# Kernel tuning notes

Measured on AMD Instinct MI355X. Metric: run time of the kernel, lower is better.

## Reference

```python
import jax, jax.numpy as jnp
import numpy as np

N_SEND = 49152   # 12 * 64^2 HEALPix nodes
N_REC = 65536    # 256x256 receiver grid
N_EDGES = 262144 # N_REC * 4 nearest senders
D_MODEL = 256
EDGE_IN, EDGE_OUT = 4, 64
LIN_IN, LIN_OUT = 320, 256
B = 2


def setup_inputs() -> dict:
    key = jax.random.key(0)
    ks = jax.random.split(key, 8)
    x = jax.random.normal(ks[0], (B, N_SEND, D_MODEL), dtype=jnp.float32)
    senders = jax.random.randint(ks[1], (N_EDGES,), 0, N_SEND, dtype=jnp.int32)
    receivers = jax.random.randint(ks[2], (N_EDGES,), 0, N_REC, dtype=jnp.int32)
    edge_index = jnp.stack([senders, receivers], axis=0)
    edge_attr = jax.random.normal(ks[3], (N_EDGES, EDGE_IN), dtype=jnp.float32)
    s = lambda fan_in: 1.0 / np.sqrt(fan_in)
    return {
        "x": x,
        "edge_index": edge_index,
        "edge_attr": edge_attr,
        "ee_w1": jax.random.normal(ks[4], (EDGE_IN, EDGE_OUT), dtype=jnp.float32) * s(EDGE_IN),
        "ee_b1": jnp.zeros((EDGE_OUT,), dtype=jnp.float32),
        "ee_w2": jax.random.normal(ks[5], (EDGE_OUT, EDGE_OUT), dtype=jnp.float32) * s(EDGE_OUT),
        "ee_b2": jnp.zeros((EDGE_OUT,), dtype=jnp.float32),
        "ff_w1": jax.random.normal(ks[6], (LIN_IN, LIN_OUT), dtype=jnp.float32) * s(LIN_IN),
        "ff_b1": jnp.zeros((LIN_OUT,), dtype=jnp.float32),
        "ff_w2": jax.random.normal(ks[7], (LIN_OUT, LIN_OUT), dtype=jnp.float32) * s(LIN_OUT),
        "ff_b2": jnp.zeros((LIN_OUT,), dtype=jnp.float32),
    }


def reference(x, edge_index, edge_attr,
              ee_w1, ee_b1, ee_w2, ee_b2,
              ff_w1, ff_b1, ff_w2, ff_b2):
    senders, receivers = edge_index[0], edge_index[1]
    # edge embedder MLP: [E, edge_in] -> [E, edge_out]
    h = jax.nn.relu(edge_attr @ ee_w1 + ee_b1)
    edge_feat = h @ ee_w2 + ee_b2                       # [E, edge_out]
    # gather sender node features: [B, E, d_model]
    v_s = x[:, senders, :]
    # concat with broadcast edge features: [B, E, d_model + edge_out]
    ef = jnp.broadcast_to(edge_feat[None], (x.shape[0],) + edge_feat.shape)
    v_s_prime = jnp.concatenate([v_s, ef], axis=-1)
    # scatter-sum onto receiver nodes: [B, n_rec, lin_in]
    v_m_sum = jnp.zeros((x.shape[0], N_REC, v_s_prime.shape[-1]), dtype=x.dtype)
    v_m_sum = v_m_sum.at[:, receivers, :].add(v_s_prime)
    # g2m feedforward: [B, n_rec, lin_out]
    h2 = jax.nn.relu(v_m_sum @ ff_w1 + ff_b1)
    return h2 @ ff_w2 + ff_b2
```

## Files before the change

### kernel.cpp

```cpp
#include <hip/hip_runtime.h>
#include <hip/hip_bf16.h>

#define N_SEND 49152
#define N_REC  65536
#define N_EDGES 262144
#define D_MODEL 256
#define EDGE_IN 4
#define EDGE_OUT 64
#define LIN_IN 320
#define LIN_OUT 256
#define BATCH 2

#define GBM 64

typedef __attribute__((ext_vector_type(4))) float f32x4;
typedef __attribute__((ext_vector_type(8))) short bf16x8;

static __device__ __forceinline__ unsigned short f2bf(float f) {
    union { float f; unsigned u; } v; v.f = f;
    unsigned r = v.u + 0x7FFF + ((v.u >> 16) & 1);
    return (unsigned short)(r >> 16);
}
static __device__ __forceinline__ float bf2f(unsigned short h) {
    union { unsigned u; float f; } v; v.u = ((unsigned)h) << 16; return v.f;
}

static __device__ __forceinline__ void async_copy16(void* lds_ptr, const void* g_ptr) {
    __builtin_amdgcn_global_load_lds(
        (const __attribute__((address_space(1))) void*)g_ptr,
        (__attribute__((address_space(3))) void*)lds_ptr, 16, 0, 0);
}

__global__ __launch_bounds__(256) void prep_fused(
    const float* __restrict__ x, unsigned short* __restrict__ xb, int nconv,
    const int* __restrict__ receivers, const float* __restrict__ edge_attr,
    const float* __restrict__ ee_w1, const float* __restrict__ ee_b1,
    const float* __restrict__ ee_w2, const float* __restrict__ ee_b2,
    unsigned short* __restrict__ efs, int* __restrict__ counts,
    const float* __restrict__ w1, const float* __restrict__ w2,
    unsigned short* __restrict__ w1t, unsigned short* __restrict__ w2t)
{
    __shared__ __align__(16) unsigned short h_lds[256 * EDGE_OUT];

    const int bid = blockIdx.x;
    const int tid = threadIdx.x;

    if (bid < nconv) {
        const size_t i = ((size_t)bid * 256 + tid) * 8;
        const float4 v0 = *(const float4*)&x[i];
        const float4 v1 = *(const float4*)&x[i + 4];
        bf16x8 o;
        o[0] = (short)f2bf(v0.x); o[1] = (short)f2bf(v0.y);
        o[2] = (short)f2bf(v0.z); o[3] = (short)f2bf(v0.w);
        o[4] = (short)f2bf(v1.x); o[5] = (short)f2bf(v1.y);
        o[6] = (short)f2bf(v1.z); o[7] = (short)f2bf(v1.w);
        *(bf16x8*)&xb[i] = o;
        return;
    }
    const int b2 = bid - nconv;

    if (b2 < N_EDGES / 256) {
        const int e0 = b2 * 256;
        atomicAdd(&counts[receivers[e0 + tid]], 1);

        {
            const float4 ea = *(const float4*)&edge_attr[(size_t)(e0 + tid) * EDGE_IN];
#pragma unroll
            for (int kb = 0; kb < 8; ++kb) {
                bf16x8 hv;
#pragma unroll
                for (int j = 0; j < 8; ++j) {
                    const int k = kb * 8 + j;
                    float a = ee_b1[k];
                    a += ea.x * ee_w1[0 * EDGE_OUT + k];
                    a += ea.y * ee_w1[1 * EDGE_OUT + k];
                    a += ea.z * ee_w1[2 * EDGE_OUT + k];
                    a += ea.w * ee_w1[3 * EDGE_OUT + k];
                    hv[j] = (short)f2bf(fmaxf(a, 0.0f));
                }
                *(bf16x8*)&h_lds[tid * EDGE_OUT + ((kb ^ (tid & 7)) * 8)] = hv;
            }
        }

        const int lane = tid & 63, wave = tid >> 6;
        const int n16 = lane & 15, hi = lane >> 4;

        bf16x8 bfr[2][4];
#pragma unroll
        for (int ch = 0; ch < 2; ++ch)
#pragma unroll
            for (int c = 0; c < 4; ++c) {
                bf16x8 b;
#pragma unroll
                for (int j = 0; j < 8; ++j) {
                    const int k = ch * 32 + hi * 8 + j;
                    b[j] = (short)f2bf(ee_w2[k * EDGE_OUT + 16 * c + n16]);
                }
                bfr[ch][c] = b;
            }

        f32x4 acc[4][4];
#pragma unroll
        for (int c = 0; c < 4; ++c) {
            const float bv = ee_b2[16 * c + n16];
#pragma unroll
            for (int t = 0; t < 4; ++t) {
                acc[t][c][0] = bv; acc[t][c][1] = bv; acc[t][c][2] = bv; acc[t][c][3] = bv;
            }
        }

#pragma unroll
        for (int ch = 0; ch < 2; ++ch) {
            bf16x8 af[4];
#pragma unroll
            for (int t = 0; t < 4; ++t) {
                const int row = 64 * wave + 16 * t + n16;
                const int slot = (4 * ch + hi) ^ (row & 7);
                af[t] = *(const bf16x8*)&h_lds[row * EDGE_OUT + slot * 8];
            }
#pragma unroll
            for (int c = 0; c < 4; ++c)
#pragma unroll
                for (int t = 0; t < 4; ++t)
                    acc[t][c] = __builtin_amdgcn_mfma_f32_16x16x32_bf16(af[t], bfr[ch][c], acc[t][c], 0, 0, 0);
        }

#pragma unroll
        for (int t = 0; t < 4; ++t)
#pragma unroll
            for (int c = 0; c < 4; ++c)
#pragma unroll
                for (int r = 0; r < 4; ++r)
                    efs[(size_t)(e0 + 64 * wave + 16 * t + 4 * hi + r) * EDGE_OUT + 16 * c + n16] =
                        f2bf(acc[t][c][r]);
        return;
    }

    {
        const int t3 = (b2 - N_EDGES / 256) * 256 + tid;
        if (t3 < 256 * LIN_IN) {
            const int n = t3 / LIN_IN, k = t3 - n * LIN_IN;
            w1t[t3] = f2bf(w1[k * LIN_OUT + n]);
        } else {
            const int t2 = t3 - 256 * LIN_IN;
            if (t2 < 256 * 256) {
                const int n = t2 >> 8, k = t2 & 255;
                w2t[t2] = f2bf(w2[k * LIN_OUT + n]);
            }
        }
    }
}

__global__ __launch_bounds__(1024) void scan_kernel(
    const int* __restrict__ counts, int* __restrict__ row_ptr,
    int* __restrict__ cursor)
{
    __shared__ int sums[1024];
    const int t = threadIdx.x;
    const int4* c4 = (const int4*)(counts + t * 64);

    int s = 0;
#pragma unroll
    for (int i = 0; i < 16; ++i) { const int4 c = c4[i]; s += c.x + c.y + c.z + c.w; }
    sums[t] = s;
    __syncthreads();

    for (int off = 1; off < 1024; off <<= 1) {
        const int v = (t >= off) ? sums[t - off] : 0;
        __syncthreads();
        sums[t] += v;
        __syncthreads();
    }

    int run = sums[t] - s;
#pragma unroll
    for (int i = 0; i < 16; ++i) {
        const int4 c = c4[i];
        int4 w;
        w.x = run; w.y = run + c.x; w.z = w.y + c.y; w.w = w.z + c.z;
        run = w.w + c.w;
        ((int4*)(row_ptr + t * 64))[i] = w;
        ((int4*)(cursor + t * 64))[i] = w;
    }
    if (t == 1023) row_ptr[N_REC] = run;
}

__global__ __launch_bounds__(256) void fill_kernel(
    const int* __restrict__ senders, const int* __restrict__ receivers,
    int* __restrict__ cursor, int* __restrict__ edge_order,
    int* __restrict__ ssort)
{
    const int e = blockIdx.x * 256 + threadIdx.x;
    const int r = receivers[e];
    const int pos = atomicAdd(&cursor[r], 1);
    edge_order[pos] = e;
    ssort[pos] = senders[e];
}

__global__ __launch_bounds__(256) void gather_kernel(
    const unsigned short* __restrict__ xb,
    const unsigned short* __restrict__ efs,
    const int* __restrict__ row_ptr,
    const int* __restrict__ edge_order,
    const int* __restrict__ ssort,
    unsigned short* __restrict__ vmb)
{
    const int lane = threadIdx.x & 63;
    const int wave = threadIdx.x >> 6;
    const int r = blockIdx.x * 4 + wave;
    const int beg = row_ptr[r], end = row_ptr[r + 1];
    const int half = lane >> 5, l2 = lane & 31;
    const size_t xbase = (size_t)half * N_SEND * D_MODEL;

    float ax[8] = {0, 0, 0, 0, 0, 0, 0, 0};
    float ae[8] = {0, 0, 0, 0, 0, 0, 0, 0};

    for (int chunk = beg; chunk < end; chunk += 64) {
        const int n = min(64, end - chunk);
        int myidx = 0, myeidx = 0;
        if (chunk + lane < end) {
            myidx = ssort[chunk + lane];
            myeidx = edge_order[chunk + lane];
        }
        for (int i = 0; i < n; i += 4) {
            bf16x8 vx[4], ve[4];
#pragma unroll
            for (int u = 0; u < 4; ++u) {
                const int s = __shfl(myidx, i + u);
                const int e = __shfl(myeidx, i + u);
                const bool p = (i + u < n);
                const bf16x8 z = {0, 0, 0, 0, 0, 0, 0, 0};
                vx[u] = z; ve[u] = z;
                if (p) vx[u] = *(const bf16x8*)&xb[xbase + (size_t)s * D_MODEL + l2 * 8];
                if (p && lane < 8) ve[u] = *(const bf16x8*)&efs[(size_t)e * EDGE_OUT + lane * 8];
            }
#pragma unroll
            for (int u = 0; u < 4; ++u)
#pragma unroll
                for (int j = 0; j < 8; ++j)
                    ax[j] += bf2f((unsigned short)vx[u][j]);
            if (lane < 8) {
#pragma unroll
                for (int u = 0; u < 4; ++u)
#pragma unroll
                    for (int j = 0; j < 8; ++j)
                        ae[j] += bf2f((unsigned short)ve[u][j]);
            }
        }
    }

    bf16x8 o;
#pragma unroll
    for (int j = 0; j < 8; ++j) o[j] = (short)f2bf(ax[j]);
    *(bf16x8*)&vmb[((size_t)(half * N_REC + r)) * LIN_IN + l2 * 8] = o;
    if (lane < 8) {
        bf16x8 oe;
#pragma unroll
        for (int j = 0; j < 8; ++j) oe[j] = (short)f2bf(ae[j]);
        *(bf16x8*)&vmb[((size_t)r) * LIN_IN + D_MODEL + lane * 8] = oe;
        *(bf16x8*)&vmb[((size_t)(N_REC + r)) * LIN_IN + D_MODEL + lane * 8] = oe;
    }
}

__global__ __launch_bounds__(256, 2) void node_mlp_fused(
    const unsigned short* __restrict__ vmb,
    const unsigned short* __restrict__ w1t,
    const float* __restrict__ b1,
    const unsigned short* __restrict__ w2t,
    const float* __restrict__ b2,
    float* __restrict__ out)
{
    __shared__ __align__(16) char lds[73728];

    const int tid  = threadIdx.x;
    const int lane = tid & 63, wc = tid >> 6;
    const int n16  = lane & 15, hi = lane >> 4;
    const size_t row0 = (size_t)blockIdx.x * GBM;
    char* const wB = lds + 40960 + wc * 8192;

    const int f_l = (n16 & 3) ^ ((n16 >> 2) & 3);
    const int hsl = (hi ^ f_l) << 4;

    auto stageA = [&](int kc) {
        const int row = tid >> 2;
        const int sl = (tid & 3) ^ ((row & 3) ^ ((row >> 2) & 3));
        const unsigned short* g = vmb + (row0 + row) * LIN_IN + kc * 32 + sl * 8;
        char* l = lds + (kc << 12) + ((tid >> 6) << 10);
        async_copy16(l, g);
    };
    auto issueB = [&](const unsigned short* BT, int ldk, int kk, int buf) {
#pragma unroll
        for (int p = 0; p < 4; ++p) {
            const int i = p * 64 + lane;
            const int row = i >> 2;
            const int sl = (i & 3) ^ ((row & 3) ^ ((row >> 2) & 3));
            const unsigned short* g = BT + (size_t)(64 * wc + row) * ldk + kk + sl * 8;
            char* l = wB + (buf << 12) + (p << 10);
            async_copy16(l, g);
        }
    };

#pragma unroll
    for (int kc = 0; kc < LIN_IN / 32; ++kc) stageA(kc);
    issueB(w1t, LIN_IN, 0, 0);
    __syncthreads();

    f32x4 acc[4][4];
#pragma unroll
    for (int c = 0; c < 4; ++c) {
        const float bv = b1[64 * wc + 16 * c + n16];
#pragma unroll
        for (int t = 0; t < 4; ++t) {
            acc[t][c][0] = bv; acc[t][c][1] = bv; acc[t][c][2] = bv; acc[t][c][3] = bv;
        }
    }

    int buf = 0;
    for (int step = 0; step < LIN_IN / 32; ++step) {
        if (step + 1 < LIN_IN / 32) {
            issueB(w1t, LIN_IN, (step + 1) * 32, buf ^ 1);
            __builtin_amdgcn_sched_barrier(0);
            asm volatile("s_waitcnt vmcnt(4)" ::: "memory");
        } else {
            asm volatile("s_waitcnt vmcnt(0)" ::: "memory");
        }
        __builtin_amdgcn_sched_barrier(0);

        bf16x8 af[4], bf[4];
        const char* Ab = lds + (step << 12);
        const char* Bb = wB + (buf << 12);
#pragma unroll
        for (int t = 0; t < 4; ++t)
            af[t] = *(const bf16x8*)(Ab + (16 * t + n16) * 64 + hsl);
#pragma unroll
        for (int c = 0; c < 4; ++c)
            bf[c] = *(const bf16x8*)(Bb + (16 * c + n16) * 64 + hsl);
#pragma unroll
        for (int c = 0; c < 4; ++c)
#pragma unroll
            for (int t = 0; t < 4; ++t)
                acc[t][c] = __builtin_amdgcn_mfma_f32_16x16x32_bf16(af[t], bf[c], acc[t][c], 0, 0, 0);
        buf ^= 1;
    }

    __syncthreads();

    issueB(w2t, LIN_OUT, 0, 0);

#pragma unroll
    for (int t = 0; t < 4; ++t)
#pragma unroll
        for (int c = 0; c < 4; ++c) {
            const int col = 64 * wc + 16 * c + n16;
            const int kc = col >> 5;
            const int b  = (col & 31) * 2;
            const int gslot = b >> 4;
#pragma unroll
            for (int r = 0; r < 4; ++r) {
                const int lrow = 16 * t + 4 * hi + r;
                const int f = (lrow & 3) ^ ((lrow >> 2) & 3);
                *(unsigned short*)(lds + (kc << 12) + lrow * 64 + (((gslot ^ f) << 4) | (b & 15))) =
                    f2bf(fmaxf(acc[t][c][r], 0.0f));
            }
        }
    asm volatile("s_waitcnt lgkmcnt(0)" ::: "memory");
    __builtin_amdgcn_s_barrier();
    __builtin_amdgcn_sched_barrier(0);

    f32x4 acc2[4][4];
#pragma unroll
    for (int c = 0; c < 4; ++c) {
        const float bv = b2[64 * wc + 16 * c + n16];
#pragma unroll
        for (int t = 0; t < 4; ++t) {
            acc2[t][c][0] = bv; acc2[t][c][1] = bv; acc2[t][c][2] = bv; acc2[t][c][3] = bv;
        }
    }

    buf = 0;
    for (int step = 0; step < LIN_OUT / 32; ++step) {
        if (step + 1 < LIN_OUT / 32) {
            issueB(w2t, LIN_OUT, (step + 1) * 32, buf ^ 1);
            __builtin_amdgcn_sched_barrier(0);
            asm volatile("s_waitcnt vmcnt(4)" ::: "memory");
        } else {
            asm volatile("s_waitcnt vmcnt(0)" ::: "memory");
        }
        __builtin_amdgcn_sched_barrier(0);

        bf16x8 af[4], bf[4];
        const char* Hb = lds + (step << 12);
        const char* Bb = wB + (buf << 12);
#pragma unroll
        for (int t = 0; t < 4; ++t)
            af[t] = *(const bf16x8*)(Hb + (16 * t + n16) * 64 + hsl);
#pragma unroll
        for (int c = 0; c < 4; ++c)
            bf[c] = *(const bf16x8*)(Bb + (16 * c + n16) * 64 + hsl);
#pragma unroll
        for (int c = 0; c < 4; ++c)
#pragma unroll
            for (int t = 0; t < 4; ++t)
                acc2[t][c] = __builtin_amdgcn_mfma_f32_16x16x32_bf16(af[t], bf[c], acc2[t][c], 0, 0, 0);
        buf ^= 1;
    }

#pragma unroll
    for (int t = 0; t < 4; ++t)
#pragma unroll
        for (int c = 0; c < 4; ++c)
#pragma unroll
            for (int r = 0; r < 4; ++r)
                out[(row0 + 16 * t + 4 * hi + r) * LIN_OUT + 64 * wc + 16 * c + n16] =
                    acc2[t][c][r];
}

extern "C" void kernel_launch(void* const* d_in, const int* in_sizes, int n_in,
                              void* d_out, int out_size, void* d_ws, size_t ws_size,
                              hipStream_t stream) {
    const float* x         = (const float*)d_in[0];
    const int*   edge_idx  = (const int*)d_in[1];
    const float* edge_attr = (const float*)d_in[2];
    const float* ee_w1     = (const float*)d_in[3];
    const float* ee_b1     = (const float*)d_in[4];
    const float* ee_w2     = (const float*)d_in[5];
    const float* ee_b2     = (const float*)d_in[6];
    const float* ff_w1     = (const float*)d_in[7];
    const float* ff_b1     = (const float*)d_in[8];
    const float* ff_w2     = (const float*)d_in[9];
    const float* ff_b2     = (const float*)d_in[10];
    float* out = (float*)d_out;

    const int* senders   = edge_idx;
    const int* receivers = edge_idx + N_EDGES;

    char* ws = (char*)d_ws;
    size_t off = 0;
    auto alloc = [&](size_t bytes) { char* p = ws + off; off += (bytes + 511) & ~511ull; return p; };

    unsigned short* vmb = (unsigned short*)alloc((size_t)BATCH * N_REC * LIN_IN * 2);
    unsigned short* efs = (unsigned short*)alloc((size_t)N_EDGES * EDGE_OUT * 2);
    unsigned short* xb  = (unsigned short*)alloc((size_t)BATCH * N_SEND * D_MODEL * 2);
    unsigned short* w1t = (unsigned short*)alloc((size_t)256 * LIN_IN * 2);
    unsigned short* w2t = (unsigned short*)alloc((size_t)256 * LIN_OUT * 2);
    int* row_ptr        = (int*)alloc((size_t)(N_REC + 1) * 4);
    int* counts         = (int*)alloc((size_t)N_REC * 4);
    int* cursor         = (int*)alloc((size_t)N_REC * 4);
    int* edge_order     = (int*)alloc((size_t)N_EDGES * 4);
    int* ssort          = (int*)alloc((size_t)N_EDGES * 4);

    hipMemsetAsync(counts, 0, (size_t)N_REC * 4, stream);

    const int nconv = (int)((size_t)BATCH * N_SEND * D_MODEL / 8 / 256);
    const int prep_grid = nconv + N_EDGES / 256 + (256 * LIN_IN + 256 * LIN_OUT + 255) / 256;
    prep_fused<<<prep_grid, 256, 0, stream>>>(
        x, xb, nconv, receivers, edge_attr, ee_w1, ee_b1, ee_w2, ee_b2,
        efs, counts, ff_w1, ff_w2, w1t, w2t);

    scan_kernel<<<1, 1024, 0, stream>>>(counts, row_ptr, cursor);

    fill_kernel<<<N_EDGES / 256, 256, 0, stream>>>(
        senders, receivers, cursor, edge_order, ssort);

    gather_kernel<<<N_REC / 4, 256, 0, stream>>>(
        xb, efs, row_ptr, edge_order, ssort, vmb);

    node_mlp_fused<<<(BATCH * N_REC) / GBM, 256, 0, stream>>>(
        vmb, w1t, ff_b1, w2t, ff_b2, out);
}
```

Measured before the change: 238.0 us.

## Apply first FF layer to sender nodes before gather, split edge-feature term

Uses linearity of the scatter-sum to multiply x by the node part of W1 per sender (98K rows) before gathering, instead of per receiver (131K rows). The edge-feature sum is now stored once per receiver rather than duplicated per batch, and its 64-column W1 slice is applied inside the node MLP kernel. The partial sum is then added to the pre-accumulated gathered value in LDS before ReLU. This cuts first-layer FLOPs and the vmb write/read traffic. The cost is an extra bf16 rounding of the projected features before summation and a separate weight-prep launch.

```diff
diff --git a/kernel.cpp b/kernel.cpp
--- a/kernel.cpp
+++ b/kernel.cpp
@@ -12,6 +12,7 @@
 #define BATCH 2
 
 #define GBM 64
+#define UGRID ((BATCH * N_SEND) / GBM)
 
 typedef __attribute__((ext_vector_type(4))) float f32x4;
 typedef __attribute__((ext_vector_type(8))) short bf16x8;
@@ -31,35 +32,110 @@
         (__attribute__((address_space(3))) void*)lds_ptr, 16, 0, 0);
 }
 
-__global__ __launch_bounds__(256) void prep_fused(
-    const float* __restrict__ x, unsigned short* __restrict__ xb, int nconv,
+__global__ __launch_bounds__(256) void wprep(
+    const float* __restrict__ w1, const float* __restrict__ w2,
+    unsigned short* __restrict__ w1xt, unsigned short* __restrict__ w1et,
+    unsigned short* __restrict__ w2t)
+{
+    const int tid = blockIdx.x * 256 + threadIdx.x;
+    if (tid < 65536) {
+        const int n = tid >> 8, k = tid & 255;
+        w1xt[tid] = f2bf(w1[k * LIN_OUT + n]);
+    } else if (tid < 65536 + 16384) {
+        const int t = tid - 65536;
+        const int n = t >> 6, k = t & 63;
+        w1et[t] = f2bf(w1[(D_MODEL + k) * LIN_OUT + n]);
+    } else if (tid < 65536 + 16384 + 65536) {
+        const int t = tid - 81920;
+        const int n = t >> 8, k = t & 255;
+        w2t[t] = f2bf(w2[k * LIN_OUT + n]);
+    }
+}
+
+__global__ __launch_bounds__(256) void prep2(
+    const float* __restrict__ x, unsigned short* __restrict__ u,
+    const unsigned short* __restrict__ w1xt,
     const int* __restrict__ receivers, const float* __restrict__ edge_attr,
     const float* __restrict__ ee_w1, const float* __restrict__ ee_b1,
     const float* __restrict__ ee_w2, const float* __restrict__ ee_b2,
-    unsigned short* __restrict__ efs, int* __restrict__ counts,
-    const float* __restrict__ w1, const float* __restrict__ w2,
-    unsigned short* __restrict__ w1t, unsigned short* __restrict__ w2t)
+    unsigned short* __restrict__ efs, int* __restrict__ counts)
 {
-    __shared__ __align__(16) unsigned short h_lds[256 * EDGE_OUT];
+    __shared__ __align__(16) char smem[32768];
 
     const int bid = blockIdx.x;
     const int tid = threadIdx.x;
 
-    if (bid < nconv) {
-        const size_t i = ((size_t)bid * 256 + tid) * 8;
-        const float4 v0 = *(const float4*)&x[i];
-        const float4 v1 = *(const float4*)&x[i + 4];
-        bf16x8 o;
-        o[0] = (short)f2bf(v0.x); o[1] = (short)f2bf(v0.y);
-        o[2] = (short)f2bf(v0.z); o[3] = (short)f2bf(v0.w);
-        o[4] = (short)f2bf(v1.x); o[5] = (short)f2bf(v1.y);
-        o[6] = (short)f2bf(v1.z); o[7] = (short)f2bf(v1.w);
-        *(bf16x8*)&xb[i] = o;
+    if (bid < UGRID) {
+        const int lane = tid & 63, wc = tid >> 6;
+        const int n16 = lane & 15, hi = lane >> 4;
+        const size_t row0 = (size_t)bid * GBM;
+
+        auto stageAx = [&](int kc, int buf) {
+#pragma unroll
+            for (int p = 0; p < 2; ++p) {
+                const int i = p * 256 + tid;
+                const int r = i >> 3, s8 = i & 7;
+                const float* g = x + (row0 + r) * D_MODEL + kc * 32 + ((s8 ^ (r & 7)) << 2);
+                char* l = smem + (buf << 13) + (p << 12) + ((tid >> 6) << 10);
+                async_copy16(l, g);
+            }
+        };
+
+        f32x4 acc[4][4];
+#pragma unroll
+        for (int c = 0; c < 4; ++c)
+#pragma unroll
+            for (int t = 0; t < 4; ++t) {
+                acc[t][c][0] = 0.f; acc[t][c][1] = 0.f; acc[t][c][2] = 0.f; acc[t][c][3] = 0.f;
+            }
+
+        stageAx(0, 0);
+        int cur = 0;
+        for (int step = 0; step < D_MODEL / 32; ++step) {
+            __syncthreads();
+            if (step + 1 < D_MODEL / 32) stageAx(step + 1, cur ^ 1);
+
+            bf16x8 bf[4];
+#pragma unroll
+            for (int c = 0; c < 4; ++c)
+                bf[c] = *(const bf16x8*)&w1xt[(size_t)(64 * wc + 16 * c + n16) * D_MODEL + step * 32 + hi * 8];
+
+            bf16x8 af[4];
+            const char* Ab = smem + (cur << 13);
+#pragma unroll
+            for (int t = 0; t < 4; ++t) {
+                const char* base = Ab + (16 * t + n16) * 128;
+                const f32x4 u0 = *(const f32x4*)(base + (((2 * hi + 0) ^ (n16 & 7)) << 4));
+                const f32x4 u1 = *(const f32x4*)(base + (((2 * hi + 1) ^ (n16 & 7)) << 4));
+                bf16x8 a;
+                a[0] = (short)f2bf(u0[0]); a[1] = (short)f2bf(u0[1]);
+                a[2] = (short)f2bf(u0[2]); a[3] = (short)f2bf(u0[3]);
+                a[4] = (short)f2bf(u1[0]); a[5] = (short)f2bf(u1[1]);
+                a[6] = (short)f2bf(u1[2]); a[7] = (short)f2bf(u1[3]);
+                af[t] = a;
+            }
+#pragma unroll
+            for (int c = 0; c < 4; ++c)
+#pragma unroll
+                for (int t = 0; t < 4; ++t)
+                    acc[t][c] = __builtin_amdgcn_mfma_f32_16x16x32_bf16(af[t], bf[c], acc[t][c], 0, 0, 0);
+            cur ^= 1;
+        }
+
+#pragma unroll
+        for (int t = 0; t < 4; ++t)
+#pragma unroll
+            for (int c = 0; c < 4; ++c)
+#pragma unroll
+                for (int r = 0; r < 4; ++r)
+                    u[(row0 + 16 * t + 4 * hi + r) * D_MODEL + 64 * wc + 16 * c + n16] =
+                        f2bf(acc[t][c][r]);
         return;
     }
-    const int b2 = bid - nconv;
-
-    if (b2 < N_EDGES / 256) {
+    const int b2 = bid - UGRID;
+
+    {
+        unsigned short* h_lds = (unsigned short*)smem;
         const int e0 = b2 * 256;
         atomicAdd(&counts[receivers[e0 + tid]], 1);
 
@@ -133,21 +209,6 @@
                 for (int r = 0; r < 4; ++r)
                     efs[(size_t)(e0 + 64 * wave + 16 * t + 4 * hi + r) * EDGE_OUT + 16 * c + n16] =
                         f2bf(acc[t][c][r]);
-        return;
-    }
-
-    {
-        const int t3 = (b2 - N_EDGES / 256) * 256 + tid;
-        if (t3 < 256 * LIN_IN) {
-            const int n = t3 / LIN_IN, k = t3 - n * LIN_IN;
-            w1t[t3] = f2bf(w1[k * LIN_OUT + n]);
-        } else {
-            const int t2 = t3 - 256 * LIN_IN;
-            if (t2 < 256 * 256) {
-                const int n = t2 >> 8, k = t2 & 255;
-                w2t[t2] = f2bf(w2[k * LIN_OUT + n]);
-            }
-        }
     }
 }
 
@@ -198,12 +259,13 @@
 }
 
 __global__ __launch_bounds__(256) void gather_kernel(
-    const unsigned short* __restrict__ xb,
+    const unsigned short* __restrict__ u,
     const unsigned short* __restrict__ efs,
     const int* __restrict__ row_ptr,
     const int* __restrict__ edge_order,
     const int* __restrict__ ssort,
-    unsigned short* __restrict__ vmb)
+    unsigned short* __restrict__ usum,
+    unsigned short* __restrict__ efsum)
 {
     const int lane = threadIdx.x & 63;
     const int wave = threadIdx.x >> 6;
@@ -225,26 +287,26 @@
         for (int i = 0; i < n; i += 4) {
             bf16x8 vx[4], ve[4];
 #pragma unroll
-            for (int u = 0; u < 4; ++u) {
-                const int s = __shfl(myidx, i + u);
-                const int e = __shfl(myeidx, i + u);
-                const bool p = (i + u < n);
+            for (int uu = 0; uu < 4; ++uu) {
+                const int s = __shfl(myidx, i + uu);
+                const int e = __shfl(myeidx, i + uu);
+                const bool p = (i + uu < n);
                 const bf16x8 z = {0, 0, 0, 0, 0, 0, 0, 0};
-                vx[u] = z; ve[u] = z;
-                if (p) vx[u] = *(const bf16x8*)&xb[xbase + (size_t)s * D_MODEL + l2 * 8];
-                if (p && lane < 8) ve[u] = *(const bf16x8*)&efs[(size_t)e * EDGE_OUT + lane * 8];
-            }
-#pragma unroll
-            for (int u = 0; u < 4; ++u)
+                vx[uu] = z; ve[uu] = z;
+                if (p) vx[uu] = *(const bf16x8*)&u[xbase + (size_t)s * D_MODEL + l2 * 8];
+                if (p && lane < 8) ve[uu] = *(const bf16x8*)&efs[(size_t)e * EDGE_OUT + lane * 8];
+            }
+#pragma unroll
+            for (int uu = 0; uu < 4; ++uu)
 #pragma unroll
                 for (int j = 0; j < 8; ++j)
-                    ax[j] += bf2f((unsigned short)vx[u][j]);
+                    ax[j] += bf2f((unsigned short)vx[uu][j]);
             if (lane < 8) {
 #pragma unroll
-                for (int u = 0; u < 4; ++u)
+                for (int uu = 0; uu < 4; ++uu)
 #pragma unroll
                     for (int j = 0; j < 8; ++j)
-                        ae[j] += bf2f((unsigned short)ve[u][j]);
+                        ae[j] += bf2f((unsigned short)ve[uu][j]);
             }
         }
     }
@@ -252,19 +314,19 @@
     bf16x8 o;
 #pragma unroll
     for (int j = 0; j < 8; ++j) o[j] = (short)f2bf(ax[j]);
-    *(bf16x8*)&vmb[((size_t)(half * N_REC + r)) * LIN_IN + l2 * 8] = o;
+    *(bf16x8*)&usum[((size_t)(half * N_REC + r)) * D_MODEL + l2 * 8] = o;
     if (lane < 8) {
         bf16x8 oe;
 #pragma unroll
         for (int j = 0; j < 8; ++j) oe[j] = (short)f2bf(ae[j]);
-        *(bf16x8*)&vmb[((size_t)r) * LIN_IN + D_MODEL + lane * 8] = oe;
-        *(bf16x8*)&vmb[((size_t)(N_REC + r)) * LIN_IN + D_MODEL + lane * 8] = oe;
+        *(bf16x8*)&efsum[(size_t)r * EDGE_OUT + lane * 8] = oe;
     }
 }
 
 __global__ __launch_bounds__(256, 2) void node_mlp_fused(
-    const unsigned short* __restrict__ vmb,
-    const unsigned short* __restrict__ w1t,
+    const unsigned short* __restrict__ usum,
+    const unsigned short* __restrict__ efsum,
+    const unsigned short* __restrict__ w1et,
     const float* __restrict__ b1,
     const unsigned short* __restrict__ w2t,
     const float* __restrict__ b2,
@@ -276,17 +338,30 @@
     const int lane = tid & 63, wc = tid >> 6;
     const int n16  = lane & 15, hi = lane >> 4;
     const size_t row0 = (size_t)blockIdx.x * GBM;
+    const int rbase = (int)(row0 & (N_REC - 1));
+    char* const ebase = lds + 32768;
     char* const wB = lds + 40960 + wc * 8192;
 
     const int f_l = (n16 & 3) ^ ((n16 >> 2) & 3);
     const int hsl = (hi ^ f_l) << 4;
 
-    auto stageA = [&](int kc) {
+    auto stageU = [&](int kc) {
         const int row = tid >> 2;
         const int sl = (tid & 3) ^ ((row & 3) ^ ((row >> 2) & 3));
-        const unsigned short* g = vmb + (row0 + row) * LIN_IN + kc * 32 + sl * 8;
+        const unsigned short* g = usum + (row0 + row) * D_MODEL + kc * 32 + sl * 8;
         char* l = lds + (kc << 12) + ((tid >> 6) << 10);
         async_copy16(l, g);
+    };
+    auto stageE = [&]() {
+#pragma unroll
+        for (int p = 0; p < 2; ++p) {
+            const int i = p * 256 + tid;
+            const int kc = i >> 8, r = (i >> 2) & 63, s = i & 3;
+            const int sl = s ^ ((r & 3) ^ ((r >> 2) & 3));
+            const unsigned short* g = efsum + (size_t)(rbase + r) * EDGE_OUT + kc * 32 + sl * 8;
+            char* l = ebase + (p << 12) + ((tid >> 6) << 10);
+            async_copy16(l, g);
+        }
     };
     auto issueB = [&](const unsigned short* BT, int ldk, int kk, int buf) {
 #pragma unroll
@@ -301,8 +376,8 @@
     };
 
 #pragma unroll
-    for (int kc = 0; kc < LIN_IN / 32; ++kc) stageA(kc);
-    issueB(w1t, LIN_IN, 0, 0);
+    for (int kc = 0; kc < 8; ++kc) stageU(kc);
+    stageE();
     __syncthreads();
 
     f32x4 acc[4][4];
@@ -315,35 +390,22 @@
         }
     }
 
-    int buf = 0;
-    for (int step = 0; step < LIN_IN / 32; ++step) {
-        if (step + 1 < LIN_IN / 32) {
-            issueB(w1t, LIN_IN, (step + 1) * 32, buf ^ 1);
-            __builtin_amdgcn_sched_barrier(0);
-            asm volatile("s_waitcnt vmcnt(4)" ::: "memory");
-        } else {
-            asm volatile("s_waitcnt vmcnt(0)" ::: "memory");
-        }
-        __builtin_amdgcn_sched_barrier(0);
-
-        bf16x8 af[4], bf[4];
-        const char* Ab = lds + (step << 12);
-        const char* Bb = wB + (buf << 12);
+#pragma unroll
+    for (int ec = 0; ec < 2; ++ec) {
+        bf16x8 bf[4];
+#pragma unroll
+        for (int c = 0; c < 4; ++c)
+            bf[c] = *(const bf16x8*)&w1et[(size_t)(64 * wc + 16 * c + n16) * EDGE_OUT + ec * 32 + hi * 8];
+        bf16x8 af[4];
 #pragma unroll
         for (int t = 0; t < 4; ++t)
-            af[t] = *(const bf16x8*)(Ab + (16 * t + n16) * 64 + hsl);
-#pragma unroll
-        for (int c = 0; c < 4; ++c)
-            bf[c] = *(const bf16x8*)(Bb + (16 * c + n16) * 64 + hsl);
+            af[t] = *(const bf16x8*)(ebase + (ec << 12) + (16 * t + n16) * 64 + hsl);
 #pragma unroll
         for (int c = 0; c < 4; ++c)
 #pragma unroll
             for (int t = 0; t < 4; ++t)
                 acc[t][c] = __builtin_amdgcn_mfma_f32_16x16x32_bf16(af[t], bf[c], acc[t][c], 0, 0, 0);
-        buf ^= 1;
-    }
-
-    __syncthreads();
+    }
 
     issueB(w2t, LIN_OUT, 0, 0);
 
@@ -359,8 +421,8 @@
             for (int r = 0; r < 4; ++r) {
                 const int lrow = 16 * t + 4 * hi + r;
                 const int f = (lrow & 3) ^ ((lrow >> 2) & 3);
-                *(unsigned short*)(lds + (kc << 12) + lrow * 64 + (((gslot ^ f) << 4) | (b & 15))) =
-                    f2bf(fmaxf(acc[t][c][r], 0.0f));
+                unsigned short* p = (unsigned short*)(lds + (kc << 12) + lrow * 64 + (((gslot ^ f) << 4) | (b & 15)));
+                *p = f2bf(fmaxf(acc[t][c][r] + bf2f(*p), 0.0f));
             }
         }
     asm volatile("s_waitcnt lgkmcnt(0)" ::: "memory");
@@ -377,7 +439,7 @@
         }
     }
 
-    buf = 0;
+    int buf = 0;
     for (int step = 0; step < LIN_OUT / 32; ++step) {
         if (step + 1 < LIN_OUT / 32) {
             issueB(w2t, LIN_OUT, (step + 1) * 32, buf ^ 1);
@@ -438,24 +500,25 @@
     size_t off = 0;
     auto alloc = [&](size_t bytes) { char* p = ws + off; off += (bytes + 511) & ~511ull; return p; };
 
-    unsigned short* vmb = (unsigned short*)alloc((size_t)BATCH * N_REC * LIN_IN * 2);
-    unsigned short* efs = (unsigned short*)alloc((size_t)N_EDGES * EDGE_OUT * 2);
-    unsigned short* xb  = (unsigned short*)alloc((size_t)BATCH * N_SEND * D_MODEL * 2);
-    unsigned short* w1t = (unsigned short*)alloc((size_t)256 * LIN_IN * 2);
-    unsigned short* w2t = (unsigned short*)alloc((size_t)256 * LIN_OUT * 2);
-    int* row_ptr        = (int*)alloc((size_t)(N_REC + 1) * 4);
-    int* counts         = (int*)alloc((size_t)N_REC * 4);
-    int* cursor         = (int*)alloc((size_t)N_REC * 4);
-    int* edge_order     = (int*)alloc((size_t)N_EDGES * 4);
-    int* ssort          = (int*)alloc((size_t)N_EDGES * 4);
+    unsigned short* usum  = (unsigned short*)alloc((size_t)BATCH * N_REC * D_MODEL * 2);
+    unsigned short* efs   = (unsigned short*)alloc((size_t)N_EDGES * EDGE_OUT * 2);
+    unsigned short* u     = (unsigned short*)alloc((size_t)BATCH * N_SEND * D_MODEL * 2);
+    unsigned short* efsum = (unsigned short*)alloc((size_t)N_REC * EDGE_OUT * 2);
+    unsigned short* w1xt  = (unsigned short*)alloc((size_t)256 * D_MODEL * 2);
+    unsigned short* w1et  = (unsigned short*)alloc((size_t)256 * EDGE_OUT * 2);
+    unsigned short* w2t   = (unsigned short*)alloc((size_t)256 * LIN_OUT * 2);
+    int* row_ptr          = (int*)alloc((size_t)(N_REC + 1) * 4);
+    int* counts           = (int*)alloc((size_t)N_REC * 4);
+    int* cursor           = (int*)alloc((size_t)N_REC * 4);
+    int* edge_order       = (int*)alloc((size_t)N_EDGES * 4);
+    int* ssort            = (int*)alloc((size_t)N_EDGES * 4);
 
     hipMemsetAsync(counts, 0, (size_t)N_REC * 4, stream);
 
-    const int nconv = (int)((size_t)BATCH * N_SEND * D_MODEL / 8 / 256);
-    const int prep_grid = nconv + N_EDGES / 256 + (256 * LIN_IN + 256 * LIN_OUT + 255) / 256;
-    prep_fused<<<prep_grid, 256, 0, stream>>>(
-        x, xb, nconv, receivers, edge_attr, ee_w1, ee_b1, ee_w2, ee_b2,
-        efs, counts, ff_w1, ff_w2, w1t, w2t);
+    wprep<<<576, 256, 0, stream>>>(ff_w1, ff_w2, w1xt, w1et, w2t);
+
+    prep2<<<UGRID + N_EDGES / 256, 256, 0, stream>>>(
+        x, u, w1xt, receivers, edge_attr, ee_w1, ee_b1, ee_w2, ee_b2, efs, counts);
 
     scan_kernel<<<1, 1024, 0, stream>>>(counts, row_ptr, cursor);
 
@@ -463,8 +526,8 @@
         senders, receivers, cursor, edge_order, ssort);
 
     gather_kernel<<<N_REC / 4, 256, 0, stream>>>(
-        xb, efs, row_ptr, edge_order, ssort, vmb);
+        u, efs, row_ptr, edge_order, ssort, usum, efsum);
 
     node_mlp_fused<<<(BATCH * N_REC) / GBM, 256, 0, stream>>>(
-        vmb, w1t, ff_b1, w2t, ff_b2, out);
-}
+        usum, efsum, w1et, ff_b1, w2t, ff_b2, out);
+}
```

Result: slower. 245.0 us (+2.9%).
